# Performance work log

Hardware: AMD Instinct MI355X
Metric: run time of the kernel (lower is better)

Reference implementation:

```python
import math
import jax, jax.numpy as jnp
import numpy as np

B, N, D = 4, 4096, 1024
H, DH = 16, 64  # D == H * DH


def setup_inputs() -> dict:
    key = jax.random.key(0)
    ks = jax.random.split(key, 7)
    s = 1.0 / math.sqrt(D)
    return {
        "tens": jax.random.normal(ks[0], (B, N, D), dtype=jnp.float32),
        "Wq": jax.random.normal(ks[1], (D, D), dtype=jnp.float32) * s,
        "bq": jax.random.normal(ks[2], (D,), dtype=jnp.float32) * 0.01,
        "Wk": jax.random.normal(ks[3], (D, D), dtype=jnp.float32) * s,
        "bk": jax.random.normal(ks[4], (D,), dtype=jnp.float32) * 0.01,
        "Wv": jax.random.normal(ks[5], (D, D), dtype=jnp.float32) * s,
        "bv": jax.random.normal(ks[6], (D,), dtype=jnp.float32) * 0.01,
    }


def reference(tens, Wq, bq, Wk, bk, Wv, bv):
    b, n, d = tens.shape
    # projections (torch Linear: x @ W^T + b)
    q = (tens @ Wq.T + bq).reshape(b, n, H, DH)  # [B,N,H,DH]
    k = (tens @ Wk.T + bk).reshape(b, n, H, DH)
    v = (tens @ Wv.T + bv).reshape(b, n, H, DH)
    scale = (1.0 / math.sqrt(DH)) / math.sqrt(n)
    # No softmax between QK^T and V => linear, reassociate as Q @ (K^T V)
    # to avoid the O(N^2) attention matrix; identical math.
    ktv = jnp.einsum("bnhd,bnhe->bhde", k, v)          # [B,H,DH,DH]
    out = jnp.einsum("bnhd,bhde->bnhe", q, ktv) * scale  # [B,N,H,DH]
    return out.reshape(b, n, d)
```

## Files before the change

### kernel.cpp

```cpp
#include <hip/hip_runtime.h>

typedef unsigned short ushort_t;
typedef __attribute__((ext_vector_type(8))) __bf16 bf16x8;
typedef __attribute__((ext_vector_type(8))) unsigned short ushort8;
typedef __attribute__((ext_vector_type(4))) unsigned short ushort4_t;
typedef __attribute__((ext_vector_type(4))) float floatx4;

__device__ inline unsigned short f2bf(float f) {
  union { float f; unsigned u; } x; x.f = f;
  return (unsigned short)((x.u + 0x7FFFu + ((x.u >> 16) & 1u)) >> 16);
}
__device__ inline float bf2f(unsigned short v) {
  union { unsigned u; float f; } x; x.u = (unsigned)v << 16;
  return x.f;
}

__global__ void cvt_tr(const float* __restrict__ tens, ushort_t* __restrict__ Xbf,
                       ushort_t* __restrict__ XT) {
  int b = blockIdx.z;
  int d0 = blockIdx.x * 64;
  int n0 = blockIdx.y * 64;
  __shared__ ushort_t sT[64 * 72];
  int t = threadIdx.x;
  int nl = t >> 2, c16 = (t & 3) * 16;
  const float* src = tens + ((long)b << 22) + (long)(n0 + nl) * 1024 + d0 + c16;
  ushort8 o0, o1;
#pragma unroll
  for (int j = 0; j < 2; ++j) {
    float4 v0 = *(const float4*)(src + j * 8);
    float4 v1 = *(const float4*)(src + j * 8 + 4);
    ushort8 o;
    o[0] = f2bf(v0.x); o[1] = f2bf(v0.y); o[2] = f2bf(v0.z); o[3] = f2bf(v0.w);
    o[4] = f2bf(v1.x); o[5] = f2bf(v1.y); o[6] = f2bf(v1.z); o[7] = f2bf(v1.w);
#pragma unroll
    for (int i = 0; i < 8; ++i) sT[(c16 + j * 8 + i) * 72 + nl] = o[i];
    if (j == 0) o0 = o; else o1 = o;
  }
  ushort_t* xdst = Xbf + ((long)b << 22) + (long)(n0 + nl) * 1024 + d0 + c16;
  *(ushort8*)xdst = o0;
  *(ushort8*)(xdst + 8) = o1;
  __syncthreads();
  int dl = t >> 2, n16 = (t & 3) * 16;
  ushort8 t0 = *(const ushort8*)(sT + dl * 72 + n16);
  ushort8 t1 = *(const ushort8*)(sT + dl * 72 + n16 + 8);
  ushort_t* dst = XT + ((long)b << 22) + (long)(d0 + dl) * 4096 + n0 + n16;
  *(ushort8*)dst = t0;
  *(ushort8*)(dst + 8) = t1;
}

__global__ void cvt2_f32_bf16(const float* __restrict__ a, ushort_t* __restrict__ oa,
                              const float* __restrict__ b, ushort_t* __restrict__ ob) {
  int id = blockIdx.x;
  const float* in; ushort_t* out;
  if (id < 512) { in = a; out = oa; } else { in = b; out = ob; id -= 512; }
  int i = (id * 256 + threadIdx.x) * 8;
  const float4* p = (const float4*)(in + i);
  float4 x = p[0], y = p[1];
  ushort8 o;
  o[0] = f2bf(x.x); o[1] = f2bf(x.y); o[2] = f2bf(x.z); o[3] = f2bf(x.w);
  o[4] = f2bf(y.x); o[5] = f2bf(y.y); o[6] = f2bf(y.z); o[7] = f2bf(y.w);
  *(ushort8*)(out + i) = o;
}

__device__ inline void gload_lds16(const void* g, void* l) {
  __builtin_amdgcn_global_load_lds(
      (const __attribute__((address_space(1))) unsigned int*)g,
      (__attribute__((address_space(3))) unsigned int*)l, 16, 0, 0);
}

__device__ inline void store_out(float* p, float v) { *p = v; }
__device__ inline void store_out(ushort_t* p, float v) { *p = f2bf(v); }

template <int K, bool BIAS, typename OutT>
__global__ void gemm_bt(const ushort_t* __restrict__ A, const ushort_t* __restrict__ Bm,
                        const float* __restrict__ bias, OutT* __restrict__ C,
                        int N, long sA_, long sB_, long sBias_, long sC_) {
  int gx = gridDim.x, gxy = gridDim.x * gridDim.y;
  int flat = blockIdx.x + gx * blockIdx.y + gxy * blockIdx.z;
  int total = gxy * gridDim.z;
  int per = total >> 3;
  int nf = (flat & 7) * per + (flat >> 3);
  int bz = nf / gxy; int rem = nf - bz * gxy;
  int by = rem / gx; int bx = rem - by * gx;

  A += (long)bz * sA_; Bm += (long)bz * sB_; C += (long)bz * sC_;
  if (BIAS) bias += (long)bz * sBias_;

  __shared__ ushort_t sA[2][128 * 32];
  __shared__ ushort_t sB[2][128 * 32];

  int t = threadIdx.x;
  int w = t >> 6, l = t & 63;
  int wy = w >> 1, wx = w & 1;
  int quad = l >> 4, m16 = l & 15;
  int mBase = by * 128, nBase = bx * 128;

  int r = l >> 2, pk = l & 3;
  int sCol = (pk ^ ((r >> 1) & 3)) * 8;
  int sRow0 = w * 32 + r;
  const ushort_t* gA0 = A + (long)(mBase + sRow0) * K + sCol;
  const ushort_t* gA1 = gA0 + 16 * K;
  const ushort_t* gB0 = Bm + (long)(nBase + sRow0) * K + sCol;
  const ushort_t* gB1 = gB0 + 16 * K;
  int lOff0 = (w * 2) * 512;
  int lOff1 = lOff0 + 512;

  int swzR = (m16 >> 1) & 3;
  int aOff = (wy * 64 + m16) * 32 + (quad ^ swzR) * 8;
  int bOff = (wx * 64 + m16) * 32 + (quad ^ swzR) * 8;

  floatx4 acc[4][4] = {};
  const int NS = K / 32;

  gload_lds16(gA0, sA[0] + lOff0);
  gload_lds16(gA1, sA[0] + lOff1);
  gload_lds16(gB0, sB[0] + lOff0);
  gload_lds16(gB1, sB[0] + lOff1);
  __syncthreads();

  for (int kt = 0; kt < NS; ++kt) {
    if (kt + 1 < NS) {
      int nb = (kt + 1) & 1, ko = (kt + 1) * 32;
      gload_lds16(gA0 + ko, sA[nb] + lOff0);
      gload_lds16(gA1 + ko, sA[nb] + lOff1);
      gload_lds16(gB0 + ko, sB[nb] + lOff0);
      gload_lds16(gB1 + ko, sB[nb] + lOff1);
    }
    __builtin_amdgcn_sched_barrier(0);
    const ushort_t* pa = sA[kt & 1];
    const ushort_t* pbm = sB[kt & 1];
    bf16x8 af[4], bfr[4];
#pragma unroll
    for (int i = 0; i < 4; ++i) af[i] = *(const bf16x8*)(pa + aOff + i * 16 * 32);
#pragma unroll
    for (int i = 0; i < 4; ++i) bfr[i] = *(const bf16x8*)(pbm + bOff + i * 16 * 32);
#pragma unroll
    for (int mi = 0; mi < 4; ++mi)
#pragma unroll
      for (int ni = 0; ni < 4; ++ni)
        acc[mi][ni] = __builtin_amdgcn_mfma_f32_16x16x32_bf16(af[mi], bfr[ni], acc[mi][ni], 0, 0, 0);
    if (kt + 1 < NS) __syncthreads();
  }

#pragma unroll
  for (int ni = 0; ni < 4; ++ni) {
    int n = nBase + wx * 64 + ni * 16 + m16;
    float bb = 0.f;
    if (BIAS) bb = bias[n];
#pragma unroll
    for (int mi = 0; mi < 4; ++mi) {
      int m0 = mBase + wy * 64 + mi * 16 + quad * 4;
      floatx4 v = acc[mi][ni];
#pragma unroll
      for (int rr = 0; rr < 4; ++rr)
        store_out(&C[(long)(m0 + rr) * N + n], v[rr] + bb);
    }
  }
}

template <int K, bool SYM, typename OutT>
__global__ void gemm64(const ushort_t* __restrict__ A, const ushort_t* __restrict__ Bm,
                       OutT* __restrict__ C, int N, long sA_, long sB_, long sC_) {
  int bz, byy, bxx;
  if (SYM) {
    int flat = blockIdx.x + gridDim.x * blockIdx.y;
    int per = (gridDim.x * gridDim.y) >> 3;
    int nf = (flat & 7) * per + (flat >> 3);
    bz = nf / 136;
    int tri = nf - bz * 136;
    byy = (int)((__fsqrt_rn(8.0f * tri + 1.0f) - 1.0f) * 0.5f);
    while ((byy + 1) * (byy + 2) / 2 <= tri) ++byy;
    while (byy * (byy + 1) / 2 > tri) --byy;
    bxx = tri - byy * (byy + 1) / 2;
  } else {
    int gx = gridDim.x, gxy = gridDim.x * gridDim.y;
    int flat = blockIdx.x + gx * blockIdx.y + gxy * blockIdx.z;
    int total = gxy * gridDim.z;
    int per = total >> 3;
    int nf = (flat & 7) * per + (flat >> 3);
    bz = nf / gxy; int rem = nf - bz * gxy;
    byy = rem / gx; bxx = rem - byy * gx;
  }

  A += (long)bz * sA_; Bm += (long)bz * sB_; C += (long)bz * sC_;

  __shared__ ushort_t sA[2][64 * 32];
  __shared__ ushort_t sB[2][64 * 32];

  int t = threadIdx.x;
  int w = t >> 6, l = t & 63;
  int wy = w >> 1, wx = w & 1;
  int quad = l >> 4, m16 = l & 15;
  int mBase = byy * 64, nBase = bxx * 64;

  int r = l >> 2, pk = l & 3;
  int sCol = (pk ^ ((r >> 1) & 3)) * 8;
  int sRow = w * 16 + r;
  const ushort_t* gA = A + (long)(mBase + sRow) * K + sCol;
  const ushort_t* gB = Bm + (long)(nBase + sRow) * K + sCol;
  int lOff = w * 512;

  int swzR = (m16 >> 1) & 3;
  int aOff = (wy * 32 + m16) * 32 + (quad ^ swzR) * 8;
  int bOff = (wx * 32 + m16) * 32 + (quad ^ swzR) * 8;

  floatx4 acc[2][2] = {};
  const int NS = K / 32;

  gload_lds16(gA, sA[0] + lOff);
  gload_lds16(gB, sB[0] + lOff);
  __syncthreads();

  for (int kt = 0; kt < NS; ++kt) {
    if (kt + 1 < NS) {
      int nb = (kt + 1) & 1, ko = (kt + 1) * 32;
      gload_lds16(gA + ko, sA[nb] + lOff);
      gload_lds16(gB + ko, sB[nb] + lOff);
    }
    __builtin_amdgcn_sched_barrier(0);
    const ushort_t* pa = sA[kt & 1];
    const ushort_t* pbm = sB[kt & 1];
    bf16x8 af[2], bfr[2];
#pragma unroll
    for (int i = 0; i < 2; ++i) af[i] = *(const bf16x8*)(pa + aOff + i * 16 * 32);
#pragma unroll
    for (int i = 0; i < 2; ++i) bfr[i] = *(const bf16x8*)(pbm + bOff + i * 16 * 32);
#pragma unroll
    for (int mi = 0; mi < 2; ++mi)
#pragma unroll
      for (int ni = 0; ni < 2; ++ni)
        acc[mi][ni] = __builtin_amdgcn_mfma_f32_16x16x32_bf16(af[mi], bfr[ni], acc[mi][ni], 0, 0, 0);
    if (kt + 1 < NS) __syncthreads();
  }

#pragma unroll
  for (int ni = 0; ni < 2; ++ni) {
    int n = nBase + wx * 32 + ni * 16 + m16;
#pragma unroll
    for (int mi = 0; mi < 2; ++mi) {
      int m0 = mBase + wy * 32 + mi * 16 + quad * 4;
      floatx4 v = acc[mi][ni];
#pragma unroll
      for (int rr = 0; rr < 4; ++rr)
        store_out(&C[(long)(m0 + rr) * N + n], v[rr]);
      if (SYM) {
        if (byy != bxx) {
          ushort4_t pkv;
#pragma unroll
          for (int rr = 0; rr < 4; ++rr) pkv[rr] = f2bf(v[rr]);
          *(ushort4_t*)((ushort_t*)C + (long)n * N + m0) = pkv;
        }
      }
    }
  }
}

__global__ void colsum(const ushort_t* __restrict__ X, float* __restrict__ s) {
  int b = blockIdx.x & 3, chunk = blockIdx.x >> 2;
  int t = threadIdx.x;
  int c8 = chunk * 32 + (t & 3) * 8;
  int ng = t >> 2;
  const ushort_t* base = X + ((long)b << 22) + c8;
  float a[8] = {};
  for (int n = ng; n < 4096; n += 64) {
    ushort8 v = *(const ushort8*)(base + (long)n * 1024);
#pragma unroll
    for (int i = 0; i < 8; ++i) a[i] += bf2f(v[i]);
  }
  __shared__ float sP[64 * 32];
#pragma unroll
  for (int i = 0; i < 8; ++i) sP[ng * 32 + (t & 3) * 8 + i] = a[i];
  __syncthreads();
  if (t < 32) {
    float acc = 0.f;
    for (int g = 0; g < 64; ++g) acc += sP[g * 32 + t];
    s[b * 1024 + chunk * 32 + t] = acc;
  }
}

__global__ void uw_kernel(const ushort_t* __restrict__ Wkbf, const ushort_t* __restrict__ Wvbf,
                          const float* __restrict__ s, float* __restrict__ u,
                          float* __restrict__ wv_s) {
  int id = blockIdx.x;
  int b = id & 3, which = (id >> 2) & 1, chunk = id >> 3;
  const ushort_t* W = which ? Wvbf : Wkbf;
  float* o = which ? wv_s : u;
  __shared__ float ss[1024];
  int t = threadIdx.x;
  *(float4*)(ss + t * 4) = *(const float4*)(s + b * 1024 + t * 4);
  __syncthreads();
  int r = chunk * 256 + t;
  const ushort_t* row = W + (long)r * 1024;
  float acc = 0.f;
  for (int k = 0; k < 1024; k += 8) {
    ushort8 v = *(const ushort8*)(row + k);
#pragma unroll
    for (int i = 0; i < 8; ++i) acc += bf2f(v[i]) * ss[k + i];
  }
  o[b * 1024 + r] = acc;
}

__global__ void make_w2(const ushort_t* __restrict__ T1, const ushort_t* __restrict__ Wvbf,
                        const float* __restrict__ u, const float* __restrict__ wv_s,
                        const float* __restrict__ bk, const float* __restrict__ bv,
                        const float* __restrict__ Wq, const float* __restrict__ bq,
                        ushort_t* __restrict__ W2T, float* __restrict__ bias2, float scale) {
  int bh = blockIdx.x, cq = blockIdx.y;
  int b = bh >> 4, h = bh & 15;
  __shared__ float sKTV[64 * 64];
  __shared__ float sW[64 * 64];
  int t = threadIdx.x, w = t >> 6, l = t & 63;
  int quad = l >> 4, m16 = l & 15;

  const ushort_t* Arow = T1 + ((long)b << 20) + (long)(h * 64 + w * 16 + m16) * 1024 + quad * 8;
  const ushort_t* Brow = Wvbf + (long)(h * 64 + m16) * 1024 + quad * 8;
  floatx4 acc[4] = {};
  for (int kt = 0; kt < 1024; kt += 32) {
    bf16x8 af = *(const bf16x8*)(Arow + kt);
#pragma unroll
    for (int j = 0; j < 4; ++j) {
      bf16x8 bfv = *(const bf16x8*)(Brow + (long)j * 16 * 1024 + kt);
      acc[j] = __builtin_amdgcn_mfma_f32_16x16x32_bf16(af, bfv, acc[j], 0, 0, 0);
    }
  }
#pragma unroll
  for (int j = 0; j < 4; ++j) {
    int e = j * 16 + m16;
    float bve = bv[h * 64 + e];
    float wse = wv_s[b * 1024 + h * 64 + e] + 4096.f * bve;
#pragma unroll
    for (int rr = 0; rr < 4; ++rr) {
      int d = w * 16 + quad * 4 + rr;
      float corr = u[b * 1024 + h * 64 + d] * bve + bk[h * 64 + d] * wse;
      sKTV[d * 64 + e] = acc[j][rr] + corr;
    }
  }
  __syncthreads();

  if (cq == 0 && t < 64) {
    float s = 0.f;
    for (int d = 0; d < 64; ++d) s += bq[h * 64 + d] * sKTV[d * 64 + t];
    bias2[b * 1024 + h * 64 + t] = s * scale;
  }

  int e = t >> 2, c0 = (t & 3) * 16;
  for (int ct = cq * 256; ct < cq * 256 + 256; ct += 64) {
    __syncthreads();
    {
      int d = t >> 2, cc = (t & 3) * 16;
#pragma unroll
      for (int j = 0; j < 16; j += 4)
        *(float4*)(sW + d * 64 + cc + j) =
            *(const float4*)(Wq + (long)(h * 64 + d) * 1024 + ct + cc + j);
    }
    __syncthreads();
    float outv[16] = {};
    for (int d = 0; d < 64; ++d) {
      float kv = sKTV[d * 64 + e];
#pragma unroll
      for (int j = 0; j < 16; ++j) outv[j] += sW[d * 64 + c0 + j] * kv;
    }
    ushort8 o0, o1;
#pragma unroll
    for (int j = 0; j < 8; ++j) { o0[j] = f2bf(outv[j] * scale); o1[j] = f2bf(outv[8 + j] * scale); }
    ushort_t* dst = W2T + ((long)(b * 1024 + h * 64 + e)) * 1024 + ct + c0;
    *(ushort8*)dst = o0;
    *(ushort8*)(dst + 8) = o1;
  }
}

extern "C" void kernel_launch(void* const* d_in, const int* in_sizes, int n_in,
                              void* d_out, int out_size, void* d_ws, size_t ws_size,
                              hipStream_t stream) {
  (void)in_sizes; (void)n_in; (void)out_size; (void)ws_size;
  const float* tens = (const float*)d_in[0];
  const float* Wq = (const float*)d_in[1];
  const float* bq = (const float*)d_in[2];
  const float* Wk = (const float*)d_in[3];
  const float* bk = (const float*)d_in[4];
  const float* Wv = (const float*)d_in[5];
  const float* bv = (const float*)d_in[6];
  float* out = (float*)d_out;

  char* w = (char*)d_ws;
  ushort_t* Xbf  = (ushort_t*)(w);
  ushort_t* XT   = (ushort_t*)(w + 33554432);
  ushort_t* Wkbf = (ushort_t*)(w + 67108864);
  ushort_t* Wvbf = (ushort_t*)(w + 69206016);
  ushort_t* Gbf  = (ushort_t*)(w + 71303168);
  ushort_t* T1   = (ushort_t*)(w + 79691776);
  float*    s    = (float*)(w + 88080384);
  float*    u    = (float*)(w + 88096768);
  float*    wv_s = (float*)(w + 88113152);
  ushort_t* W2T  = (ushort_t*)(w + 89178112);
  float*    bias2= (float*)(w + 97566720);

  const float scale = (1.0f / 8.0f) / 64.0f;

  hipLaunchKernelGGL(cvt_tr, dim3(16, 64, 4), dim3(256), 0, stream, tens, Xbf, XT);
  hipLaunchKernelGGL(cvt2_f32_bf16, dim3(1024), dim3(256), 0, stream, Wk, Wkbf, Wv, Wvbf);
  hipLaunchKernelGGL(colsum, dim3(128), dim3(256), 0, stream, Xbf, s);

  hipLaunchKernelGGL((gemm64<4096, true, ushort_t>), dim3(136, 4, 1), dim3(256), 0, stream,
                     XT, XT, Gbf, 1024, 4194304L, 4194304L, 1048576L);

  hipLaunchKernelGGL(uw_kernel, dim3(32), dim3(256), 0, stream, Wkbf, Wvbf, s, u, wv_s);

  hipLaunchKernelGGL((gemm64<1024, false, ushort_t>), dim3(16, 16, 4), dim3(256), 0, stream,
                     Wkbf, Gbf, T1, 1024, 0L, 1048576L, 1048576L);

  hipLaunchKernelGGL(make_w2, dim3(64, 4), dim3(256), 0, stream,
                     T1, Wvbf, u, wv_s, bk, bv, Wq, bq, W2T, bias2, scale);

  hipLaunchKernelGGL((gemm_bt<1024, true, float>), dim3(8, 32, 4), dim3(256), 0, stream,
                     Xbf, W2T, bias2, out, 1024,
                     4194304L, 1048576L, 1024L, 4194304L);
}
```

Baseline: 328.4 us.

## Fuse weight conversion and column sums into transpose kernel; deepen GEMM k-step

New measurement: 293.2 us. 10.7% less time.

```diff
diff --git a/kernel.cpp b/kernel.cpp
--- a/kernel.cpp
+++ b/kernel.cpp
@@ -16,12 +16,27 @@
 }
 
 __global__ void cvt_tr(const float* __restrict__ tens, ushort_t* __restrict__ Xbf,
-                       ushort_t* __restrict__ XT) {
+                       ushort_t* __restrict__ XT, float* __restrict__ s,
+                       const float* __restrict__ Wk, ushort_t* __restrict__ Wkbf,
+                       const float* __restrict__ Wv, ushort_t* __restrict__ Wvbf) {
+  int t = threadIdx.x;
+  if (blockIdx.z == 4) {
+    int flat = blockIdx.x + 16 * blockIdx.y;
+    const float* in; ushort_t* out;
+    if (flat < 512) { in = Wk; out = Wkbf; } else { in = Wv; out = Wvbf; flat -= 512; }
+    int i = (flat * 256 + t) * 8;
+    const float4* p = (const float4*)(in + i);
+    float4 x = p[0], y = p[1];
+    ushort8 o;
+    o[0] = f2bf(x.x); o[1] = f2bf(x.y); o[2] = f2bf(x.z); o[3] = f2bf(x.w);
+    o[4] = f2bf(y.x); o[5] = f2bf(y.y); o[6] = f2bf(y.z); o[7] = f2bf(y.w);
+    *(ushort8*)(out + i) = o;
+    return;
+  }
   int b = blockIdx.z;
   int d0 = blockIdx.x * 64;
   int n0 = blockIdx.y * 64;
   __shared__ ushort_t sT[64 * 72];
-  int t = threadIdx.x;
   int nl = t >> 2, c16 = (t & 3) * 16;
   const float* src = tens + ((long)b << 22) + (long)(n0 + nl) * 1024 + d0 + c16;
   ushort8 o0, o1;
@@ -46,20 +61,12 @@
   ushort_t* dst = XT + ((long)b << 22) + (long)(d0 + dl) * 4096 + n0 + n16;
   *(ushort8*)dst = t0;
   *(ushort8*)(dst + 8) = t1;
-}
-
-__global__ void cvt2_f32_bf16(const float* __restrict__ a, ushort_t* __restrict__ oa,
-                              const float* __restrict__ b, ushort_t* __restrict__ ob) {
-  int id = blockIdx.x;
-  const float* in; ushort_t* out;
-  if (id < 512) { in = a; out = oa; } else { in = b; out = ob; id -= 512; }
-  int i = (id * 256 + threadIdx.x) * 8;
-  const float4* p = (const float4*)(in + i);
-  float4 x = p[0], y = p[1];
-  ushort8 o;
-  o[0] = f2bf(x.x); o[1] = f2bf(x.y); o[2] = f2bf(x.z); o[3] = f2bf(x.w);
-  o[4] = f2bf(y.x); o[5] = f2bf(y.y); o[6] = f2bf(y.z); o[7] = f2bf(y.w);
-  *(ushort8*)(out + i) = o;
+  float ps = 0.f;
+#pragma unroll
+  for (int i = 0; i < 8; ++i) ps += bf2f(t0[i]) + bf2f(t1[i]);
+  ps += __shfl_xor(ps, 1);
+  ps += __shfl_xor(ps, 2);
+  if ((t & 3) == 0) atomicAdd(&s[b * 1024 + d0 + dl], ps);
 }
 
 __device__ inline void gload_lds16(const void* g, void* l) {
@@ -184,8 +191,8 @@
 
   A += (long)bz * sA_; Bm += (long)bz * sB_; C += (long)bz * sC_;
 
-  __shared__ ushort_t sA[2][64 * 32];
-  __shared__ ushort_t sB[2][64 * 32];
+  __shared__ ushort_t sA[2][2][64 * 32];
+  __shared__ ushort_t sB[2][2][64 * 32];
 
   int t = threadIdx.x;
   int w = t >> 6, l = t & 63;
@@ -205,31 +212,42 @@
   int bOff = (wx * 32 + m16) * 32 + (quad ^ swzR) * 8;
 
   floatx4 acc[2][2] = {};
-  const int NS = K / 32;
-
-  gload_lds16(gA, sA[0] + lOff);
-  gload_lds16(gB, sB[0] + lOff);
+  const int NS = K / 64;
+
+#pragma unroll
+  for (int kk = 0; kk < 2; ++kk) {
+    gload_lds16(gA + kk * 32, sA[0][kk] + lOff);
+    gload_lds16(gB + kk * 32, sB[0][kk] + lOff);
+  }
   __syncthreads();
 
   for (int kt = 0; kt < NS; ++kt) {
     if (kt + 1 < NS) {
-      int nb = (kt + 1) & 1, ko = (kt + 1) * 32;
-      gload_lds16(gA + ko, sA[nb] + lOff);
-      gload_lds16(gB + ko, sB[nb] + lOff);
+      int nb = (kt + 1) & 1, ko = (kt + 1) * 64;
+#pragma unroll
+      for (int kk = 0; kk < 2; ++kk) {
+        gload_lds16(gA + ko + kk * 32, sA[nb][kk] + lOff);
+        gload_lds16(gB + ko + kk * 32, sB[nb][kk] + lOff);
+      }
     }
     __builtin_amdgcn_sched_barrier(0);
-    const ushort_t* pa = sA[kt & 1];
-    const ushort_t* pbm = sB[kt & 1];
-    bf16x8 af[2], bfr[2];
-#pragma unroll
-    for (int i = 0; i < 2; ++i) af[i] = *(const bf16x8*)(pa + aOff + i * 16 * 32);
-#pragma unroll
-    for (int i = 0; i < 2; ++i) bfr[i] = *(const bf16x8*)(pbm + bOff + i * 16 * 32);
-#pragma unroll
-    for (int mi = 0; mi < 2; ++mi)
-#pragma unroll
-      for (int ni = 0; ni < 2; ++ni)
-        acc[mi][ni] = __builtin_amdgcn_mfma_f32_16x16x32_bf16(af[mi], bfr[ni], acc[mi][ni], 0, 0, 0);
+    int cb = kt & 1;
+    bf16x8 af[2][2], bfr[2][2];
+#pragma unroll
+    for (int kk = 0; kk < 2; ++kk) {
+#pragma unroll
+      for (int i = 0; i < 2; ++i) {
+        af[i][kk] = *(const bf16x8*)(sA[cb][kk] + aOff + i * 16 * 32);
+        bfr[i][kk] = *(const bf16x8*)(sB[cb][kk] + bOff + i * 16 * 32);
+      }
+    }
+#pragma unroll
+    for (int kk = 0; kk < 2; ++kk)
+#pragma unroll
+      for (int mi = 0; mi < 2; ++mi)
+#pragma unroll
+        for (int ni = 0; ni < 2; ++ni)
+          acc[mi][ni] = __builtin_amdgcn_mfma_f32_16x16x32_bf16(af[mi][kk], bfr[ni][kk], acc[mi][ni], 0, 0, 0);
     if (kt + 1 < NS) __syncthreads();
   }
 
@@ -252,29 +270,6 @@
         }
       }
     }
-  }
-}
-
-__global__ void colsum(const ushort_t* __restrict__ X, float* __restrict__ s) {
-  int b = blockIdx.x & 3, chunk = blockIdx.x >> 2;
-  int t = threadIdx.x;
-  int c8 = chunk * 32 + (t & 3) * 8;
-  int ng = t >> 2;
-  const ushort_t* base = X + ((long)b << 22) + c8;
-  float a[8] = {};
-  for (int n = ng; n < 4096; n += 64) {
-    ushort8 v = *(const ushort8*)(base + (long)n * 1024);
-#pragma unroll
-    for (int i = 0; i < 8; ++i) a[i] += bf2f(v[i]);
-  }
-  __shared__ float sP[64 * 32];
-#pragma unroll
-  for (int i = 0; i < 8; ++i) sP[ng * 32 + (t & 3) * 8 + i] = a[i];
-  __syncthreads();
-  if (t < 32) {
-    float acc = 0.f;
-    for (int g = 0; g < 64; ++g) acc += sP[g * 32 + t];
-    s[b * 1024 + chunk * 32 + t] = acc;
   }
 }
 
@@ -397,9 +392,9 @@
 
   const float scale = (1.0f / 8.0f) / 64.0f;
 
-  hipLaunchKernelGGL(cvt_tr, dim3(16, 64, 4), dim3(256), 0, stream, tens, Xbf, XT);
-  hipLaunchKernelGGL(cvt2_f32_bf16, dim3(1024), dim3(256), 0, stream, Wk, Wkbf, Wv, Wvbf);
-  hipLaunchKernelGGL(colsum, dim3(128), dim3(256), 0, stream, Xbf, s);
+  hipMemsetAsync(s, 0, 16384, stream);
+  hipLaunchKernelGGL(cvt_tr, dim3(16, 64, 5), dim3(256), 0, stream,
+                     tens, Xbf, XT, s, Wk, Wkbf, Wv, Wvbf);
 
   hipLaunchKernelGGL((gemm64<4096, true, ushort_t>), dim3(136, 4, 1), dim3(256), 0, stream,
                      XT, XT, Gbf, 1024, 4194304L, 4194304L, 1048576L);
```
